# Kernel tuning notes

Measured on AMD Instinct MI355X. Metric: run time of the kernel, lower is better.

## Reference

```python
import jax, jax.numpy as jnp
import numpy as np

ALPHA, BETA, LMBD, GAMMA = 0.0005, 1.0, 1.0, 1.0
MARGIN, THRES = 100.0, 0.5
EPS = 1e-7


def _bce(p, t):
    p = jnp.clip(p, EPS, 1.0 - EPS)
    return -jnp.mean(t * jnp.log(p) + (1.0 - t) * jnp.log1p(-p))


def setup_inputs() -> dict:
    key = jax.random.key(0)
    ks = jax.random.split(key, 9)
    B, T, D, C = 16, 2048, 2048, 100
    return {
        "score_act": jax.random.uniform(ks[0], (B, C), jnp.float32),
        "score_bkg": jax.random.uniform(ks[1], (B, C), jnp.float32),
        "feat_act": jax.random.normal(ks[2], (B, T, D), jnp.float32),
        "feat_bkg": jax.random.normal(ks[3], (B, T, D), jnp.float32),
        "label": jax.random.uniform(ks[4], (B, C), jnp.float32),
        "gt": jax.random.uniform(ks[5], (B, T, C), jnp.float32),
        "sup_cas": jax.random.uniform(ks[6], (B, T, C), jnp.float32),
        "cas_s": jax.random.uniform(ks[7], (B, T, C), jnp.float32),
        "cas_t": jax.random.uniform(ks[8], (B, T, C), jnp.float32),
    }


def reference(score_act, score_bkg, feat_act, feat_bkg, label, gt, sup_cas, cas_s, cas_t):
    # classification BCE against normalized multi-label target
    label_n = label / jnp.sum(label, axis=1, keepdims=True)
    loss_cls = _bce(score_act, label_n)

    # background BCE against uniform 1/C target
    C = label.shape[1]
    loss_be = _bce(score_bkg, jnp.full_like(label, 1.0 / C))

    # uncertainty modeling: feature-magnitude margin loss
    act_norm = jnp.linalg.norm(jnp.mean(feat_act, axis=1), axis=1)  # [B]
    bkg_norm = jnp.linalg.norm(jnp.mean(feat_bkg, axis=1), axis=1)  # [B]
    loss_act = jnp.maximum(MARGIN - act_norm, 0.0)
    loss_um = jnp.mean((loss_act + bkg_norm) ** 2)

    # balanced_ce, vectorized over (batch, class): mean of L2 norms over time
    # for (i,j) slices that contain at least one positive snippet
    pmask = (gt > THRES).astype(sup_cas.dtype)            # [B,T,C]
    norms = jnp.linalg.norm(sup_cas - pmask, axis=1)      # [B,C]
    valid = jnp.sum(pmask, axis=1) > 0                    # [B,C]
    count = jnp.maximum(jnp.sum(valid), 1).astype(norms.dtype)
    loss_sup = jnp.sum(jnp.where(valid, norms, 0.0)) / count

    # student/teacher CAS MSE
    loss_st = jnp.mean((cas_s - cas_t) ** 2)

    loss_total = (loss_cls + ALPHA * loss_um + BETA * loss_be
                  + LMBD * loss_sup + GAMMA * loss_st)
    return jnp.stack([loss_total, loss_cls, loss_be, loss_um, loss_sup, loss_st])
```

## Files before the change

### kernel.cpp

```cpp
#include <hip/hip_runtime.h>
#include <cmath>

constexpr int B = 16, T = 2048, D = 2048, C = 100;
#define EPS_F 1e-7f

typedef float v4f __attribute__((ext_vector_type(4)));

template <int ROWS>
__global__ __launch_bounds__(256) void colsum_kernel(
        const float* __restrict__ fa, const float* __restrict__ fb,
        float* __restrict__ out) {
    const int z = blockIdx.z;
    const float* feat = (z < B) ? fa : fb;
    const int b = (z < B) ? z : z - B;
    const int d0 = (blockIdx.x * 256 + threadIdx.x) * 4;
    const int t0 = blockIdx.y * ROWS;
    const float* base = feat + ((size_t)b * T + t0) * D + d0;
    v4f acc = (v4f)(0.f);
#pragma unroll 8
    for (int t = 0; t < ROWS; ++t) {
        v4f v = __builtin_nontemporal_load(
            reinterpret_cast<const v4f*>(base + (size_t)t * D));
        acc += v;
    }
    float* o = out + (size_t)z * D + d0;
    atomicAdd(o + 0, acc.x);
    atomicAdd(o + 1, acc.y);
    atomicAdd(o + 2, acc.z);
    atomicAdd(o + 3, acc.w);
}

template <int ROWS>
__global__ __launch_bounds__(256) void sup_kernel(
        const float* __restrict__ gt, const float* __restrict__ sup,
        float* __restrict__ sumsq, float* __restrict__ cnt) {
    const int b = blockIdx.y;
    const int j = threadIdx.x & 31;
    const int r = threadIdx.x >> 5;
    if (j >= C / 4) return;
    const int t0 = blockIdx.x * ROWS + r;
    size_t base = ((size_t)b * T + t0) * C + 4 * j;
    v4f acc = (v4f)(0.f);
    v4f pc  = (v4f)(0.f);
#pragma unroll
    for (int t = 0; t < ROWS; t += 8) {
        v4f g = __builtin_nontemporal_load(
            reinterpret_cast<const v4f*>(gt  + base + (size_t)t * C));
        v4f s = __builtin_nontemporal_load(
            reinterpret_cast<const v4f*>(sup + base + (size_t)t * C));
        float m, d;
        m = (g.x > 0.5f) ? 1.f : 0.f; d = s.x - m; acc.x += d * d; pc.x += m;
        m = (g.y > 0.5f) ? 1.f : 0.f; d = s.y - m; acc.y += d * d; pc.y += m;
        m = (g.z > 0.5f) ? 1.f : 0.f; d = s.z - m; acc.z += d * d; pc.z += m;
        m = (g.w > 0.5f) ? 1.f : 0.f; d = s.w - m; acc.w += d * d; pc.w += m;
    }
    float* sq = sumsq + b * C + 4 * j;
    float* ct = cnt   + b * C + 4 * j;
    atomicAdd(sq + 0, acc.x); atomicAdd(sq + 1, acc.y);
    atomicAdd(sq + 2, acc.z); atomicAdd(sq + 3, acc.w);
    atomicAdd(ct + 0, pc.x);  atomicAdd(ct + 1, pc.y);
    atomicAdd(ct + 2, pc.z);  atomicAdd(ct + 3, pc.w);
}

__global__ __launch_bounds__(256) void st_kernel(
        const float* __restrict__ s, const float* __restrict__ t,
        float* __restrict__ acc, int n4) {
    int idx = blockIdx.x * blockDim.x + threadIdx.x;
    int stride = gridDim.x * blockDim.x;
    float local = 0.f;
    for (int i = idx; i < n4; i += stride) {
        v4f a  = __builtin_nontemporal_load(
            reinterpret_cast<const v4f*>(s) + i);
        v4f b4 = __builtin_nontemporal_load(
            reinterpret_cast<const v4f*>(t) + i);
        v4f d = a - b4;
        local += d.x * d.x + d.y * d.y + d.z * d.z + d.w * d.w;
    }
    for (int off = 32; off; off >>= 1) local += __shfl_down(local, off, 64);
    __shared__ float wsum[4];
    int lane = threadIdx.x & 63, wv = threadIdx.x >> 6;
    if (lane == 0) wsum[wv] = local;
    __syncthreads();
    if (threadIdx.x == 0)
        atomicAdd(acc, wsum[0] + wsum[1] + wsum[2] + wsum[3]);
}

__device__ __forceinline__ float block_reduce(float v, float* s4) {
    for (int off = 32; off; off >>= 1) v += __shfl_down(v, off, 64);
    int lane = threadIdx.x & 63, wv = threadIdx.x >> 6;
    __syncthreads();
    if (lane == 0) s4[wv] = v;
    __syncthreads();
    return s4[0] + s4[1] + s4[2] + s4[3];
}

__global__ __launch_bounds__(256) void final_kernel(
        const float* __restrict__ score_act,
        const float* __restrict__ score_bkg,
        const float* __restrict__ label,
        const float* __restrict__ colsum,
        const float* __restrict__ sup_sumsq,
        const float* __restrict__ sup_cnt,
        const float* __restrict__ st_acc,
        float* __restrict__ out) {
    __shared__ float s4[4];
    __shared__ float rowsum[B];
    __shared__ float an[B], bn[B];
    const int tid = threadIdx.x;
    const int N = B * C;

    if (tid < B) rowsum[tid] = 0.f;
    __syncthreads();
    for (int i = tid; i < N; i += 256) atomicAdd(&rowsum[i / C], label[i]);
    __syncthreads();

    float lc = 0.f;
    for (int i = tid; i < N; i += 256) {
        float tgt = label[i] / rowsum[i / C];
        float p = fminf(fmaxf(score_act[i], EPS_F), 1.f - EPS_F);
        lc -= tgt * logf(p) + (1.f - tgt) * log1pf(-p);
    }
    float loss_cls = block_reduce(lc, s4) / (float)N;

    float lb = 0.f;
    const float u = 1.f / (float)C;
    for (int i = tid; i < N; i += 256) {
        float p = fminf(fmaxf(score_bkg[i], EPS_F), 1.f - EPS_F);
        lb -= u * logf(p) + (1.f - u) * log1pf(-p);
    }
    float loss_be = block_reduce(lb, s4) / (float)N;

    const float invT = 1.f / (float)T;
    const v4f* cs4 = reinterpret_cast<const v4f*>(colsum);
    for (int b = 0; b < B; ++b) {
        float la = 0.f, lg = 0.f;
        for (int i = tid; i < D / 4; i += 256) {
            v4f va = cs4[(size_t)b * (D / 4) + i];
            v4f vb = cs4[(size_t)(b + B) * (D / 4) + i];
            la += (va.x * va.x + va.y * va.y + va.z * va.z + va.w * va.w) * invT * invT;
            lg += (vb.x * vb.x + vb.y * vb.y + vb.z * vb.z + vb.w * vb.w) * invT * invT;
        }
        float sa = block_reduce(la, s4);
        float sb = block_reduce(lg, s4);
        if (tid == 0) { an[b] = sqrtf(sa); bn[b] = sqrtf(sb); }
    }
    __syncthreads();

    float ss = 0.f, sc = 0.f;
    for (int i = tid; i < N; i += 256) {
        if (sup_cnt[i] > 0.f) { ss += sqrtf(sup_sumsq[i]); sc += 1.f; }
    }
    float sup_sum   = block_reduce(ss, s4);
    float sup_count = block_reduce(sc, s4);

    if (tid == 0) {
        float loss_um = 0.f;
        for (int b = 0; b < B; ++b) {
            float la = fmaxf(100.f - an[b], 0.f);
            float v = la + bn[b];
            loss_um += v * v;
        }
        loss_um /= (float)B;
        float loss_sup = sup_sum / fmaxf(sup_count, 1.f);
        float loss_st = *st_acc / (float)((size_t)B * T * C);
        float total = loss_cls + 0.0005f * loss_um + 1.0f * loss_be
                    + 1.0f * loss_sup + 1.0f * loss_st;
        out[0] = total;
        out[1] = loss_cls;
        out[2] = loss_be;
        out[3] = loss_um;
        out[4] = loss_sup;
        out[5] = loss_st;
    }
}

extern "C" void kernel_launch(void* const* d_in, const int* in_sizes, int n_in,
                              void* d_out, int out_size, void* d_ws, size_t ws_size,
                              hipStream_t stream) {
    const float* score_act = (const float*)d_in[0];
    const float* score_bkg = (const float*)d_in[1];
    const float* feat_act  = (const float*)d_in[2];
    const float* feat_bkg  = (const float*)d_in[3];
    const float* label     = (const float*)d_in[4];
    const float* gt        = (const float*)d_in[5];
    const float* sup_cas   = (const float*)d_in[6];
    const float* cas_s     = (const float*)d_in[7];
    const float* cas_t     = (const float*)d_in[8];
    float* out = (float*)d_out;
    float* ws  = (float*)d_ws;

    float* colsum    = ws;
    float* sup_sumsq = ws + (size_t)2 * B * D;
    float* sup_cnt   = sup_sumsq + B * C;
    float* st_acc    = sup_cnt + B * C;
    size_t ws_needed = ((size_t)2 * B * D + 2 * B * C + 1) * sizeof(float);

    (void)hipMemsetAsync(d_ws, 0, ws_needed, stream);

    {
        constexpr int ROWS = 64;
        dim3 grid(D / (256 * 4), T / ROWS, 2 * B);
        colsum_kernel<ROWS><<<grid, 256, 0, stream>>>(feat_act, feat_bkg, colsum);
    }
    {
        constexpr int ROWS = 64;
        dim3 grid(T / ROWS, B);
        sup_kernel<ROWS><<<grid, 256, 0, stream>>>(gt, sup_cas, sup_sumsq, sup_cnt);
    }
    {
        int n4 = (B * T * C) / 4;
        st_kernel<<<1024, 256, 0, stream>>>(cas_s, cas_t, st_acc, n4);
    }
    final_kernel<<<1, 256, 0, stream>>>(score_act, score_bkg, label,
                                        colsum, sup_sumsq, sup_cnt, st_acc, out);
}
```

Before: 664.5 us.

## Fuse all reduction kernels into one launch with last-block finalization

Merges the colsum, sup, and student/teacher MSE kernels and the final scalar reduction into a single kernel. Blocks are partitioned by index across the three streaming tasks, and an atomic counter elects the last finishing block to compute the final losses. Per-block row counts double, giving fewer blocks and fewer atomics. The aim is to remove the launch gaps and tail serialization between the four kernels and let the streaming phases overlap. The cost is a threadfence/counter handshake and atomic loads in the final block, and the per-task block counts are now fixed.

```diff
diff --git a/kernel.cpp b/kernel.cpp
--- a/kernel.cpp
+++ b/kernel.cpp
@@ -4,88 +4,18 @@
 constexpr int B = 16, T = 2048, D = 2048, C = 100;
 #define EPS_F 1e-7f
 
+constexpr int COLSUM_BLOCKS = 1024;
+constexpr int SUP_BLOCKS    = 256;
+constexpr int ST_BLOCKS     = 256;
+constexpr int TOTAL_BLOCKS  = COLSUM_BLOCKS + SUP_BLOCKS + ST_BLOCKS;
+
 typedef float v4f __attribute__((ext_vector_type(4)));
 
-template <int ROWS>
-__global__ __launch_bounds__(256) void colsum_kernel(
-        const float* __restrict__ fa, const float* __restrict__ fb,
-        float* __restrict__ out) {
-    const int z = blockIdx.z;
-    const float* feat = (z < B) ? fa : fb;
-    const int b = (z < B) ? z : z - B;
-    const int d0 = (blockIdx.x * 256 + threadIdx.x) * 4;
-    const int t0 = blockIdx.y * ROWS;
-    const float* base = feat + ((size_t)b * T + t0) * D + d0;
-    v4f acc = (v4f)(0.f);
-#pragma unroll 8
-    for (int t = 0; t < ROWS; ++t) {
-        v4f v = __builtin_nontemporal_load(
-            reinterpret_cast<const v4f*>(base + (size_t)t * D));
-        acc += v;
-    }
-    float* o = out + (size_t)z * D + d0;
-    atomicAdd(o + 0, acc.x);
-    atomicAdd(o + 1, acc.y);
-    atomicAdd(o + 2, acc.z);
-    atomicAdd(o + 3, acc.w);
-}
-
-template <int ROWS>
-__global__ __launch_bounds__(256) void sup_kernel(
-        const float* __restrict__ gt, const float* __restrict__ sup,
-        float* __restrict__ sumsq, float* __restrict__ cnt) {
-    const int b = blockIdx.y;
-    const int j = threadIdx.x & 31;
-    const int r = threadIdx.x >> 5;
-    if (j >= C / 4) return;
-    const int t0 = blockIdx.x * ROWS + r;
-    size_t base = ((size_t)b * T + t0) * C + 4 * j;
-    v4f acc = (v4f)(0.f);
-    v4f pc  = (v4f)(0.f);
-#pragma unroll
-    for (int t = 0; t < ROWS; t += 8) {
-        v4f g = __builtin_nontemporal_load(
-            reinterpret_cast<const v4f*>(gt  + base + (size_t)t * C));
-        v4f s = __builtin_nontemporal_load(
-            reinterpret_cast<const v4f*>(sup + base + (size_t)t * C));
-        float m, d;
-        m = (g.x > 0.5f) ? 1.f : 0.f; d = s.x - m; acc.x += d * d; pc.x += m;
-        m = (g.y > 0.5f) ? 1.f : 0.f; d = s.y - m; acc.y += d * d; pc.y += m;
-        m = (g.z > 0.5f) ? 1.f : 0.f; d = s.z - m; acc.z += d * d; pc.z += m;
-        m = (g.w > 0.5f) ? 1.f : 0.f; d = s.w - m; acc.w += d * d; pc.w += m;
-    }
-    float* sq = sumsq + b * C + 4 * j;
-    float* ct = cnt   + b * C + 4 * j;
-    atomicAdd(sq + 0, acc.x); atomicAdd(sq + 1, acc.y);
-    atomicAdd(sq + 2, acc.z); atomicAdd(sq + 3, acc.w);
-    atomicAdd(ct + 0, pc.x);  atomicAdd(ct + 1, pc.y);
-    atomicAdd(ct + 2, pc.z);  atomicAdd(ct + 3, pc.w);
-}
-
-__global__ __launch_bounds__(256) void st_kernel(
-        const float* __restrict__ s, const float* __restrict__ t,
-        float* __restrict__ acc, int n4) {
-    int idx = blockIdx.x * blockDim.x + threadIdx.x;
-    int stride = gridDim.x * blockDim.x;
-    float local = 0.f;
-    for (int i = idx; i < n4; i += stride) {
-        v4f a  = __builtin_nontemporal_load(
-            reinterpret_cast<const v4f*>(s) + i);
-        v4f b4 = __builtin_nontemporal_load(
-            reinterpret_cast<const v4f*>(t) + i);
-        v4f d = a - b4;
-        local += d.x * d.x + d.y * d.y + d.z * d.z + d.w * d.w;
-    }
-    for (int off = 32; off; off >>= 1) local += __shfl_down(local, off, 64);
-    __shared__ float wsum[4];
-    int lane = threadIdx.x & 63, wv = threadIdx.x >> 6;
-    if (lane == 0) wsum[wv] = local;
-    __syncthreads();
-    if (threadIdx.x == 0)
-        atomicAdd(acc, wsum[0] + wsum[1] + wsum[2] + wsum[3]);
-}
-
-__device__ __forceinline__ float block_reduce(float v, float* s4) {
+__device__ __forceinline__ float aload(const float* p) {
+    return __hip_atomic_load(p, __ATOMIC_RELAXED, __HIP_MEMORY_SCOPE_AGENT);
+}
+
+__device__ __forceinline__ float block_reduce(float v, volatile float* s4) {
     for (int off = 32; off; off >>= 1) v += __shfl_down(v, off, 64);
     int lane = threadIdx.x & 63, wv = threadIdx.x >> 6;
     __syncthreads();
@@ -94,19 +24,105 @@
     return s4[0] + s4[1] + s4[2] + s4[3];
 }
 
-__global__ __launch_bounds__(256) void final_kernel(
+__global__ __launch_bounds__(256) void fused_kernel(
+        const float* __restrict__ feat_act, const float* __restrict__ feat_bkg,
+        const float* __restrict__ gt,       const float* __restrict__ sup,
+        const float* __restrict__ cas_s,    const float* __restrict__ cas_t,
         const float* __restrict__ score_act,
         const float* __restrict__ score_bkg,
         const float* __restrict__ label,
-        const float* __restrict__ colsum,
-        const float* __restrict__ sup_sumsq,
-        const float* __restrict__ sup_cnt,
-        const float* __restrict__ st_acc,
-        float* __restrict__ out) {
+        float* __restrict__ ws, float* __restrict__ out) {
+    float* colsum    = ws;
+    float* sup_sumsq = ws + (size_t)2 * B * D;
+    float* sup_cnt   = sup_sumsq + B * C;
+    float* st_acc    = sup_cnt + B * C;
+    unsigned* counter = reinterpret_cast<unsigned*>(st_acc + 1);
+
     __shared__ float s4[4];
     __shared__ float rowsum[B];
     __shared__ float an[B], bn[B];
+    __shared__ int s_last;
+
     const int tid = threadIdx.x;
+    const int bid = blockIdx.x;
+
+    if (bid < COLSUM_BLOCKS) {
+        const int z   = bid >> 5;
+        const int rem = bid & 31;
+        const int tch = rem >> 1;
+        const int xh  = rem & 1;
+        const float* feat = (z < B) ? feat_act : feat_bkg;
+        const int b  = (z < B) ? z : z - B;
+        const int d0 = (xh * 256 + tid) * 4;
+        const int t0 = tch * 128;
+        const float* base = feat + ((size_t)b * T + t0) * D + d0;
+        v4f acc = (v4f)(0.f);
+#pragma unroll 8
+        for (int t = 0; t < 128; ++t)
+            acc += __builtin_nontemporal_load(
+                reinterpret_cast<const v4f*>(base + (size_t)t * D));
+        float* o = colsum + (size_t)z * D + d0;
+        atomicAdd(o + 0, acc.x);
+        atomicAdd(o + 1, acc.y);
+        atomicAdd(o + 2, acc.z);
+        atomicAdd(o + 3, acc.w);
+    } else if (bid < COLSUM_BLOCKS + SUP_BLOCKS) {
+        const int s   = bid - COLSUM_BLOCKS;
+        const int b   = s >> 4;
+        const int tch = s & 15;
+        const int j   = tid & 31;
+        const int r   = tid >> 5;
+        if (j < C / 4) {
+            const int t0 = tch * 128 + r;
+            size_t base = ((size_t)b * T + t0) * C + 4 * j;
+            v4f acc = (v4f)(0.f);
+            v4f pc  = (v4f)(0.f);
+#pragma unroll
+            for (int t = 0; t < 128; t += 8) {
+                v4f g = __builtin_nontemporal_load(
+                    reinterpret_cast<const v4f*>(gt  + base + (size_t)t * C));
+                v4f sv = __builtin_nontemporal_load(
+                    reinterpret_cast<const v4f*>(sup + base + (size_t)t * C));
+                float m, d;
+                m = (g.x > 0.5f) ? 1.f : 0.f; d = sv.x - m; acc.x += d * d; pc.x += m;
+                m = (g.y > 0.5f) ? 1.f : 0.f; d = sv.y - m; acc.y += d * d; pc.y += m;
+                m = (g.z > 0.5f) ? 1.f : 0.f; d = sv.z - m; acc.z += d * d; pc.z += m;
+                m = (g.w > 0.5f) ? 1.f : 0.f; d = sv.w - m; acc.w += d * d; pc.w += m;
+            }
+            float* sq = sup_sumsq + b * C + 4 * j;
+            float* ct = sup_cnt   + b * C + 4 * j;
+            atomicAdd(sq + 0, acc.x); atomicAdd(sq + 1, acc.y);
+            atomicAdd(sq + 2, acc.z); atomicAdd(sq + 3, acc.w);
+            atomicAdd(ct + 0, pc.x);  atomicAdd(ct + 1, pc.y);
+            atomicAdd(ct + 2, pc.z);  atomicAdd(ct + 3, pc.w);
+        }
+    } else {
+        const int n4 = (B * T * C) / 4;
+        int idx = (bid - COLSUM_BLOCKS - SUP_BLOCKS) * 256 + tid;
+        float local = 0.f;
+        for (int i = idx; i < n4; i += ST_BLOCKS * 256) {
+            v4f a  = __builtin_nontemporal_load(
+                reinterpret_cast<const v4f*>(cas_s) + i);
+            v4f b4 = __builtin_nontemporal_load(
+                reinterpret_cast<const v4f*>(cas_t) + i);
+            v4f d = a - b4;
+            local += d.x * d.x + d.y * d.y + d.z * d.z + d.w * d.w;
+        }
+        for (int off = 32; off; off >>= 1) local += __shfl_down(local, off, 64);
+        int lane = tid & 63, wv = tid >> 6;
+        if (lane == 0) s4[wv] = local;
+        __syncthreads();
+        if (tid == 0) atomicAdd(st_acc, s4[0] + s4[1] + s4[2] + s4[3]);
+    }
+
+    __threadfence();
+    __syncthreads();
+    if (tid == 0)
+        s_last = (atomicAdd(counter, 1u) == (unsigned)(TOTAL_BLOCKS - 1)) ? 1 : 0;
+    __syncthreads();
+    if (!s_last) return;
+    __threadfence();
+
     const int N = B * C;
 
     if (tid < B) rowsum[tid] = 0.f;
@@ -131,14 +147,13 @@
     float loss_be = block_reduce(lb, s4) / (float)N;
 
     const float invT = 1.f / (float)T;
-    const v4f* cs4 = reinterpret_cast<const v4f*>(colsum);
     for (int b = 0; b < B; ++b) {
         float la = 0.f, lg = 0.f;
-        for (int i = tid; i < D / 4; i += 256) {
-            v4f va = cs4[(size_t)b * (D / 4) + i];
-            v4f vb = cs4[(size_t)(b + B) * (D / 4) + i];
-            la += (va.x * va.x + va.y * va.y + va.z * va.z + va.w * va.w) * invT * invT;
-            lg += (vb.x * vb.x + vb.y * vb.y + vb.z * vb.z + vb.w * vb.w) * invT * invT;
+        for (int d = tid; d < D; d += 256) {
+            float va = aload(colsum + (size_t)b * D + d) * invT;
+            float vb = aload(colsum + (size_t)(b + B) * D + d) * invT;
+            la += va * va;
+            lg += vb * vb;
         }
         float sa = block_reduce(la, s4);
         float sb = block_reduce(lg, s4);
@@ -148,7 +163,7 @@
 
     float ss = 0.f, sc = 0.f;
     for (int i = tid; i < N; i += 256) {
-        if (sup_cnt[i] > 0.f) { ss += sqrtf(sup_sumsq[i]); sc += 1.f; }
+        if (aload(sup_cnt + i) > 0.f) { ss += sqrtf(aload(sup_sumsq + i)); sc += 1.f; }
     }
     float sup_sum   = block_reduce(ss, s4);
     float sup_count = block_reduce(sc, s4);
@@ -162,7 +177,7 @@
         }
         loss_um /= (float)B;
         float loss_sup = sup_sum / fmaxf(sup_count, 1.f);
-        float loss_st = *st_acc / (float)((size_t)B * T * C);
+        float loss_st = aload(st_acc) / (float)((size_t)B * T * C);
         float total = loss_cls + 0.0005f * loss_um + 1.0f * loss_be
                     + 1.0f * loss_sup + 1.0f * loss_st;
         out[0] = total;
@@ -189,28 +204,10 @@
     float* out = (float*)d_out;
     float* ws  = (float*)d_ws;
 
-    float* colsum    = ws;
-    float* sup_sumsq = ws + (size_t)2 * B * D;
-    float* sup_cnt   = sup_sumsq + B * C;
-    float* st_acc    = sup_cnt + B * C;
-    size_t ws_needed = ((size_t)2 * B * D + 2 * B * C + 1) * sizeof(float);
-
+    size_t ws_needed = ((size_t)2 * B * D + 2 * B * C + 2) * sizeof(float);
     (void)hipMemsetAsync(d_ws, 0, ws_needed, stream);
 
-    {
-        constexpr int ROWS = 64;
-        dim3 grid(D / (256 * 4), T / ROWS, 2 * B);
-        colsum_kernel<ROWS><<<grid, 256, 0, stream>>>(feat_act, feat_bkg, colsum);
-    }
-    {
-        constexpr int ROWS = 64;
-        dim3 grid(T / ROWS, B);
-        sup_kernel<ROWS><<<grid, 256, 0, stream>>>(gt, sup_cas, sup_sumsq, sup_cnt);
-    }
-    {
-        int n4 = (B * T * C) / 4;
-        st_kernel<<<1024, 256, 0, stream>>>(cas_s, cas_t, st_acc, n4);
-    }
-    final_kernel<<<1, 256, 0, stream>>>(score_act, score_bkg, label,
-                                        colsum, sup_sumsq, sup_cnt, st_acc, out);
-}
+    fused_kernel<<<TOTAL_BLOCKS, 256, 0, stream>>>(
+        feat_act, feat_bkg, gt, sup_cas, cas_s, cas_t,
+        score_act, score_bkg, label, ws, out);
+}
```

Result: slower. 835.9 us (+25.8%).
